# Kernel optimization log

Hardware: AMD Instinct MI355X
Metric: run time of the kernel (lower is better)

## Reference

```python
import jax, jax.numpy as jnp
import numpy as np

GELU = lambda v: jax.nn.gelu(v, approximate=False)  # torch nn.GELU default (exact erf)


def _gconv(x, w):
    # grouped conv1d, valid padding; w: (C,1,K), groups=C. lax conv = cross-correlation, same as torch.
    return jax.lax.conv_general_dilated(x, w, (1,), [(0, 0)],
                                        dimension_numbers=('NCH', 'OIH', 'NCH'),
                                        feature_group_count=x.shape[1])


def _conv(x, w, b):
    # dense conv1d, kernel 3, padding=1
    y = jax.lax.conv_general_dilated(x, w, (1,), [(1, 1)],
                                     dimension_numbers=('NCH', 'OIH', 'NCH'))
    return y + b[None, :, None]


def setup_inputs() -> dict:
    key = jax.random.key(0)
    ks = jax.random.split(key, 12)
    B, C, L = 8, 64, 2048
    H, FL, HD, TD, level = 32, 8, 64, 16, 3
    Cs = (1 + level) * C  # 256 channels into the ODE
    n = lambda k, s: (jax.random.normal(k, s) * 0.05).astype(jnp.float32)
    z = lambda s: jnp.zeros(s, jnp.float32)
    return dict(
        x=jax.random.normal(ks[0], (B, C, L), jnp.float32),
        # DyWAN_QR params
        sw1=n(ks[1], (H, C)), sb1=z((H,)),
        sw2=n(ks[2], (H, H)), sb2=z((H,)),
        sw3=n(ks[3], (2 * FL, H)), sb3=z((2 * FL,)),
        # ODE time embed / FiLM params
        tw1=n(ks[4], (TD, 1)), tb1=z((TD,)),
        tw2=n(ks[5], (TD, TD)), tb2=z((TD,)),
        cw=n(ks[6], (2 * HD, TD)), cb=z((2 * HD,)),
        # ODE conv stack params
        k1=n(ks[7], (HD, Cs, 3)), kb1=z((HD,)),
        k2=n(ks[8], (HD, HD, 3)), kb2=z((HD,)),
        k3=n(ks[9], (Cs, HD, 3)), kb3=z((Cs,)),
    )


def reference(x, sw1, sb1, sw2, sb2, sw3, sb3, tw1, tb1, tw2, tb2, cw, cb,
              k1, kb1, k2, kb2, k3, kb3):
    B, C, L = x.shape
    level, FL, T = 3, 8, 5

    def dywan(a):
        # stat_net: adaptive max pool over L -> (B,C) -> Linear -> GELU
        feat = GELU(jnp.max(a, axis=-1) @ sw1.T + sb1)
        raw = GELU(feat @ sw2.T + sb2) @ sw3.T + sb3  # (B, 2*FL)
        lo_raw, hi_raw = raw[:, :FL], raw[:, FL:]
        # QR of an (FL,1) column vector == L2 normalization (up to LAPACK sign)
        lo = lo_raw / jnp.linalg.norm(lo_raw, axis=1, keepdims=True)
        hi = hi_raw / jnp.linalg.norm(hi_raw, axis=1, keepdims=True)
        return lo, hi

    pad = FL - 1
    coeffs = [x]
    approx = x
    for _ in range(level):
        lo, hi = dywan(approx)
        lo_f = jnp.broadcast_to(lo.mean(0)[None, None, :], (C, 1, FL))
        hi_f = jnp.broadcast_to(hi.mean(0)[None, None, :], (C, 1, FL))
        ap = jnp.pad(approx, ((0, 0), (0, 0), (pad // 2, pad - pad // 2)), mode='reflect')
        new_approx = _gconv(ap, lo_f)[..., :L]
        coeffs.append(_gconv(ap, hi_f)[..., :L])
        approx = new_approx
    stacked = jnp.concatenate(coeffs, axis=1)  # (B, (1+level)*C, L)

    def ode_f(t, y):
        te = jnp.reshape(t, (1, 1)).astype(y.dtype)
        te = GELU(te @ tw1.T + tb1) @ tw2.T + tb2          # (1, TD)
        cond = te @ cw.T + cb                               # (1, 2*HD)
        hd = cond.shape[1] // 2
        gamma, beta = cond[:, :hd], cond[:, hd:]
        h = _conv(y, k1, kb1)
        h = (1.0 + gamma[:, :, None]) * h + beta[:, :, None]  # FiLM
        h = GELU(h)
        h = GELU(_conv(h, k2, kb2))
        return _conv(h, k3, kb3)

    # dopri5 tableau, fixed grid over linspace(0, 1, T) (b7 = 0, so 6 stages)
    hs = 1.0 / (T - 1)
    y = stacked
    for i in range(T - 1):
        t0 = i * hs
        s1 = ode_f(t0, y)
        s2 = ode_f(t0 + hs / 5, y + hs * (1 / 5) * s1)
        s3 = ode_f(t0 + 3 * hs / 10, y + hs * (3 / 40 * s1 + 9 / 40 * s2))
        s4 = ode_f(t0 + 4 * hs / 5, y + hs * (44 / 45 * s1 - 56 / 15 * s2 + 32 / 9 * s3))
        s5 = ode_f(t0 + 8 * hs / 9, y + hs * (19372 / 6561 * s1 - 25360 / 2187 * s2
                                              + 64448 / 6561 * s3 - 212 / 729 * s4))
        s6 = ode_f(t0 + hs, y + hs * (9017 / 3168 * s1 - 355 / 33 * s2 + 46732 / 5247 * s3
                                      + 49 / 176 * s4 - 5103 / 18656 * s5))
        y = y + hs * (35 / 384 * s1 + 500 / 1113 * s3 + 125 / 192 * s4
                      - 2187 / 6784 * s5 + 11 / 84 * s6)
    ode_out = y

    yl = ode_out[:, :C, :]
    yh0 = ode_out[:, C:2 * C, :]
    yh1 = ode_out[:, 2 * C:3 * C, :]
    yh2 = ode_out[:, 3 * C:4 * C, :]

    dx = ode_f(jnp.float32(1.0), ode_out)
    inner = jnp.sum(stacked * dx, axis=(1, 2))  # (B,)
    ecloss = jnp.mean(inner ** 2)
    return (yl, yh0, yh1, yh2, ecloss)
```

## Files before the change

### kernel.cpp

```cpp
#include <hip/hip_runtime.h>
#include <math.h>

#define B 8
#define C 64
#define L 2048
#define CS 256
#define BCL  (B*C*L)
#define BCSL (B*CS*L)
#define HS 0.25f

typedef unsigned short u16;
typedef unsigned int   u32;
typedef __attribute__((ext_vector_type(8))) short sh8;
typedef __attribute__((ext_vector_type(4))) float f4;
typedef __attribute__((ext_vector_type(8))) unsigned short us8;
typedef __attribute__((ext_vector_type(4))) unsigned short us4;

__device__ __forceinline__ float gelu(float x) {
    return 0.5f * x * (1.0f + erff(x * 0.70710678118654752440f));
}
__device__ __forceinline__ u16 f2b(float f) {
    u32 u = __float_as_uint(f);
    u32 r = u + 0x7FFFu + ((u >> 16) & 1u);
    return (u16)(r >> 16);
}
__device__ __forceinline__ float b2f(u16 h) {
    return __uint_as_float(((u32)h) << 16);
}
__device__ __forceinline__ u32 encmax(float f) {
    u32 b = __float_as_uint(f);
    return (b & 0x80000000u) ? ~b : (b | 0x80000000u);
}
__device__ __forceinline__ float decmax(u32 u) {
    return __uint_as_float((u & 0x80000000u) ? (u ^ 0x80000000u) : ~u);
}

struct ComboB { const u16* p[6]; float c[6]; };

__global__ __launch_bounds__(256) void prep_k(const float* __restrict__ w,
        u16* __restrict__ dst, int IC, int OC) {
    int idx = blockIdx.x * 256 + threadIdx.x;
    int OCG = OC >> 4;
    int j = idx & 7, lane = (idx >> 3) & 63, t = idx >> 9;
    int ocg = t % OCG, c = t / OCG;
    int oc = ocg * 16 + (lane & 15);
    int K = c * 32 + ((lane >> 4) & 3) * 8 + j;
    int kk = K / IC, ic = K % IC;
    dst[idx] = f2b(w[((size_t)oc * IC + ic) * 3 + kk]);
}

__global__ void cond25_k(const float* __restrict__ tw1, const float* __restrict__ tb1,
                         const float* __restrict__ tw2, const float* __restrict__ tb2,
                         const float* __restrict__ cw, const float* __restrict__ cb,
                         float* __restrict__ condall) {
    __shared__ float te1[16], te2[16];
    int tix = blockIdx.x;
    int tid = threadIdx.x;
    double add[6] = {0.0, 0.25/5.0, 3.0*0.25/10.0, 4.0*0.25/5.0, 8.0*0.25/9.0, 0.25};
    float t = (tix == 24) ? 1.0f : (float)((double)(tix / 6) * 0.25 + add[tix % 6]);
    if (tid < 16) te1[tid] = gelu(t * tw1[tid] + tb1[tid]);
    __syncthreads();
    if (tid < 16) {
        float s = tb2[tid];
        for (int k = 0; k < 16; ++k) s += te1[k] * tw2[tid*16+k];
        te2[tid] = s;
    }
    __syncthreads();
    float s = cb[tid];
    for (int j = 0; j < 16; ++j) s += te2[j] * cw[tid*16+j];
    condall[tix*128 + tid] = s;
}

template<int NC, int EPI>
__global__ __launch_bounds__(512) void fused_k(ComboB in,
        const u16* __restrict__ wp1, const float* __restrict__ kb1,
        const u16* __restrict__ wp2, const float* __restrict__ kb2,
        const u16* __restrict__ wp3, const float* __restrict__ kb3,
        const float* __restrict__ condall, int tix,
        u16* __restrict__ outSb,
        float* __restrict__ y, u16* __restrict__ yb,
        float* __restrict__ outp, const float* __restrict__ stacked,
        double* __restrict__ inner)
{
    __shared__ u16 xs1[50][264];
    __shared__ u16 h1t[50][72];
    __shared__ u16 h2t[34][72];
    __shared__ u16 ypart[32][264];
    __shared__ double sred[8];
    const int tid = threadIdx.x;
    const int l0  = blockIdx.x * 32;
    const int b   = blockIdx.y;
    const int g0  = l0 - 3;

    const float cy1 = HS*(35.f/384.f), cy3 = HS*(500.f/1113.f),
                cy4 = HS*(125.f/192.f), cy5 = -HS*(2187.f/6784.f),
                cy6 = HS*(11.f/84.f);

    for (int i = tid; i < 12*264; i += 512) xs1[38 + i/264][i%264] = 0;
    if (tid < 144) h1t[48 + tid/72][tid%72] = 0;

    for (int idx = tid; idx < 38*32; idx += 512) {
        int r = idx >> 5, c8 = idx & 31;
        int gl = g0 + r;
        us8 val;
        if (gl >= 0 && gl < L) {
            size_t a = ((size_t)b * L + gl) * 256 + c8 * 8;
            us8 v0 = *(const us8*)(in.p[0] + a);
            if (NC == 1) {
                val = v0;
            } else {
                float f[8];
                float yp[8];
                #pragma unroll
                for (int j = 0; j < 8; ++j) { f[j] = b2f(v0[j]); yp[j] = 0.f; }
                #pragma unroll
                for (int t = 1; t < NC; ++t) {
                    us8 vt = *(const us8*)(in.p[t] + a);
                    #pragma unroll
                    for (int j = 0; j < 8; ++j) {
                        float bv = b2f(vt[j]);
                        f[j] += in.c[t] * bv;
                        if ((EPI == 1 || EPI == 2) && (t == 1 || t == 3 || t == 4 || t == 5)) {
                            float cy = (t == 1) ? cy1 : (t == 3) ? cy3 : (t == 4) ? cy4 : cy5;
                            yp[j] += cy * bv;
                        }
                    }
                }
                #pragma unroll
                for (int j = 0; j < 8; ++j) val[j] = f2b(f[j]);
                if ((EPI == 1 || EPI == 2) && r >= 3 && r < 35) {
                    us8 ypk;
                    #pragma unroll
                    for (int j = 0; j < 8; ++j) ypk[j] = f2b(yp[j]);
                    *(us8*)&ypart[r - 3][c8 * 8] = ypk;
                }
            }
        } else {
            #pragma unroll
            for (int j = 0; j < 8; ++j) val[j] = 0;
        }
        *(us8*)&xs1[r][c8 * 8] = val;
    }
    __syncthreads();

    const int wave = tid >> 6, lane = tid & 63;
    const int nlo = lane & 15, quad = lane >> 4;

    const int ocg12  = wave & 3;
    const int nfbase = (wave < 4) ? 0 : 2;
    const int nfcnt  = (wave < 4) ? 2 : 1;

    f4 a1[2];
    a1[0] = f4{0.f,0.f,0.f,0.f}; a1[1] = a1[0];
    {
        const sh8* w1 = (const sh8*)wp1;
        for (int c = 0; c < 24; ++c) {
            int kk = c >> 3, ic0 = (c & 7) << 5;
            sh8 A = w1[(c*4 + ocg12)*64 + lane];
            #pragma unroll
            for (int k = 0; k < 2; ++k) {
                if (k < nfcnt) {
                    int nf = nfbase + k;
                    sh8 Bv = *(const sh8*)&xs1[nf*16 + nlo + kk][ic0 + quad*8];
                    a1[k] = __builtin_amdgcn_mfma_f32_16x16x32_bf16(A, Bv, a1[k], 0, 0, 0);
                }
            }
        }
    }
    {
        const float* cd = condall + tix*128;
        const int oc0 = ocg12*16 + quad*4;
        #pragma unroll
        for (int k = 0; k < 2; ++k) {
            if (k < nfcnt) {
                int nf = nfbase + k;
                int p = nf*16 + nlo;
                int gp = l0 - 2 + p;
                bool ok = (p < 36) && (gp >= 0) && (gp < L);
                us4 pk;
                #pragma unroll
                for (int reg = 0; reg < 4; ++reg) {
                    int oc = oc0 + reg;
                    float v = (1.f + cd[oc]) * (a1[k][reg] + kb1[oc]) + cd[64+oc];
                    pk[reg] = ok ? f2b(gelu(v)) : (u16)0;
                }
                *(us4*)&h1t[p][oc0] = pk;
            }
        }
    }
    __syncthreads();

    f4 a2[2];
    a2[0] = f4{0.f,0.f,0.f,0.f}; a2[1] = a2[0];
    {
        const sh8* w2 = (const sh8*)wp2;
        #pragma unroll
        for (int c = 0; c < 6; ++c) {
            int kk = c >> 1, ic0 = (c & 1) << 5;
            sh8 A = w2[(c*4 + ocg12)*64 + lane];
            #pragma unroll
            for (int k = 0; k < 2; ++k) {
                if (k < nfcnt) {
                    int nf = nfbase + k;
                    sh8 Bv = *(const sh8*)&h1t[nf*16 + nlo + kk][ic0 + quad*8];
                    a2[k] = __builtin_amdgcn_mfma_f32_16x16x32_bf16(A, Bv, a2[k], 0, 0, 0);
                }
            }
        }
    }
    {
        const int oc0 = ocg12*16 + quad*4;
        #pragma unroll
        for (int k = 0; k < 2; ++k) {
            if (k < nfcnt) {
                int nf = nfbase + k;
                int q = nf*16 + nlo;
                if (q < 34) {
                    int gq = l0 - 1 + q;
                    bool ok = (gq >= 0) && (gq < L);
                    us4 pk;
                    #pragma unroll
                    for (int reg = 0; reg < 4; ++reg)
                        pk[reg] = ok ? f2b(gelu(a2[k][reg] + kb2[oc0 + reg])) : (u16)0;
                    *(us4*)&h2t[q][oc0] = pk;
                }
            }
        }
    }
    __syncthreads();

    f4 a3[2][2];
    #pragma unroll
    for (int mf = 0; mf < 2; ++mf) { a3[mf][0] = f4{0.f,0.f,0.f,0.f}; a3[mf][1] = a3[mf][0]; }
    {
        const sh8* w3 = (const sh8*)wp3;
        #pragma unroll
        for (int c = 0; c < 6; ++c) {
            int kk = c >> 1, ic0 = (c & 1) << 5;
            sh8 B0 = *(const sh8*)&h2t[nlo + kk][ic0 + quad*8];
            sh8 B1 = *(const sh8*)&h2t[16 + nlo + kk][ic0 + quad*8];
            #pragma unroll
            for (int mf = 0; mf < 2; ++mf) {
                sh8 A = w3[(c*16 + wave*2 + mf)*64 + lane];
                a3[mf][0] = __builtin_amdgcn_mfma_f32_16x16x32_bf16(A, B0, a3[mf][0], 0, 0, 0);
                a3[mf][1] = __builtin_amdgcn_mfma_f32_16x16x32_bf16(A, B1, a3[mf][1], 0, 0, 0);
            }
        }
    }

    if (EPI == 3) {
        double acc = 0.0;
        #pragma unroll
        for (int mf = 0; mf < 2; ++mf)
            #pragma unroll
            for (int nf = 0; nf < 2; ++nf) {
                int pos = l0 + nf*16 + nlo;
                #pragma unroll
                for (int reg = 0; reg < 4; ++reg) {
                    int oc = (wave*2 + mf)*16 + quad*4 + reg;
                    size_t idx = ((size_t)b*CS + oc)*L + pos;
                    float dx = a3[mf][nf][reg] + kb3[oc];
                    acc += (double)stacked[idx] * (double)dx;
                }
            }
        #pragma unroll
        for (int off = 32; off > 0; off >>= 1) acc += __shfl_down(acc, off, 64);
        if (lane == 0) sred[wave] = acc;
        __syncthreads();
        if (tid == 0) {
            double s = 0.0;
            #pragma unroll
            for (int w = 0; w < 8; ++w) s += sred[w];
            atomicAdd(&inner[b], s);
        }
    } else if (EPI == 0) {
        #pragma unroll
        for (int mf = 0; mf < 2; ++mf) {
            int baseoc = (wave*2 + mf)*16 + quad*4;
            #pragma unroll
            for (int nf = 0; nf < 2; ++nf) {
                int pos = l0 + nf*16 + nlo;
                us4 pk;
                #pragma unroll
                for (int reg = 0; reg < 4; ++reg)
                    pk[reg] = f2b(a3[mf][nf][reg] + kb3[baseoc + reg]);
                *(us4*)(outSb + ((size_t)b*L + pos)*256 + baseoc) = pk;
            }
        }
    } else {
        #pragma unroll
        for (int mf = 0; mf < 2; ++mf) {
            int baseoc = (wave*2 + mf)*16 + quad*4;
            #pragma unroll
            for (int nf = 0; nf < 2; ++nf) {
                int pl = nf*16 + nlo;
                int pos = l0 + pl;
                us4 yp4 = *(const us4*)&ypart[pl][baseoc];
                us4 pk;
                #pragma unroll
                for (int reg = 0; reg < 4; ++reg) {
                    int oc = baseoc + reg;
                    size_t idx = ((size_t)b*CS + oc)*L + pos;
                    float s6 = a3[mf][nf][reg] + kb3[oc];
                    float yv = y[idx] + b2f(yp4[reg]) + cy6 * s6;
                    pk[reg] = f2b(yv);
                    if (EPI == 1) y[idx] = yv;
                    if (EPI == 2) {
                        size_t oidx = (((size_t)(oc >> 6)*B + b)*64 + (oc & 63))*L + pos;
                        outp[oidx] = yv;
                    }
                }
                *(us4*)(yb + ((size_t)b*L + pos)*256 + baseoc) = pk;
            }
        }
    }
}

__global__ __launch_bounds__(256) void mlp_k(const u32* __restrict__ bm,
    const float* __restrict__ sw1, const float* __restrict__ sb1,
    const float* __restrict__ sw2, const float* __restrict__ sb2,
    const float* __restrict__ sw3, const float* __restrict__ sb3,
    float* __restrict__ filt) {
    __shared__ float m[8][64], f1[8][32], f2[8][32], raw[8][16], nrm[8][2];
    int tid = threadIdx.x;
    for (int i = tid; i < 512; i += 256) m[i >> 6][i & 63] = decmax(bm[i]);
    __syncthreads();
    {
        int b = tid >> 5, h = tid & 31;
        float s = sb1[h];
        for (int c = 0; c < 64; ++c) s += m[b][c] * sw1[h*64+c];
        f1[b][h] = gelu(s);
    }
    __syncthreads();
    {
        int b = tid >> 5, h = tid & 31;
        float s = sb2[h];
        for (int k = 0; k < 32; ++k) s += f1[b][k] * sw2[h*32+k];
        f2[b][h] = gelu(s);
    }
    __syncthreads();
    if (tid < 128) {
        int b = tid >> 4, j = tid & 15;
        float s = sb3[j];
        for (int k = 0; k < 32; ++k) s += f2[b][k] * sw3[j*32+k];
        raw[b][j] = s;
    }
    __syncthreads();
    if (tid < 16) {
        int b = tid >> 1, half = tid & 1;
        float s = 0.f;
        for (int j = 0; j < 8; ++j) { float v = raw[b][half*8+j]; s += v*v; }
        nrm[b][half] = sqrtf(s);
    }
    __syncthreads();
    if (tid < 16) {
        int half = tid >> 3;
        float s = 0.f;
        for (int b = 0; b < 8; ++b) s += raw[b][tid] / nrm[b][half];
        filt[tid] = s * 0.125f;
    }
}

__global__ __launch_bounds__(256) void wconv_k(const float* __restrict__ ap,
    const float* __restrict__ filt, float* __restrict__ apOut,
    float* __restrict__ stacked, int lev, u32* __restrict__ bmaxn) {
    __shared__ float f[16];
    __shared__ float red[256];
    if (threadIdx.x < 16) f[threadIdx.x] = filt[threadIdx.x];
    __syncthreads();
    size_t idx = (size_t)blockIdx.x * 256 + threadIdx.x;
    int l = (int)(idx & 2047);
    size_t bc = idx >> 11;
    int c = (int)(bc & 63), b = (int)(bc >> 6);
    const float* row = ap + (bc << 11);
    float lo = 0.f, hi = 0.f;
    #pragma unroll
    for (int k = 0; k < 8; ++k) {
        int mI = l + k - 3;
        mI = mI < 0 ? -mI : (mI >= L ? 2*L - 2 - mI : mI);
        float v = row[mI];
        lo += v * f[k];
        hi += v * f[8+k];
    }
    stacked[((size_t)b * CS + (size_t)(lev+1) * 64 + c) * L + l] = hi;
    if (bmaxn) {
        apOut[idx] = lo;
        red[threadIdx.x] = lo;
        __syncthreads();
        for (int s = 128; s > 0; s >>= 1) {
            if (threadIdx.x < s) red[threadIdx.x] = fmaxf(red[threadIdx.x], red[threadIdx.x + s]);
            __syncthreads();
        }
        if (threadIdx.x == 0) atomicMax(&bmaxn[blockIdx.x >> 3], encmax(red[0]));
    }
}

__global__ __launch_bounds__(256) void copyx_k(const float* __restrict__ x,
        float* __restrict__ st, u32* __restrict__ bmax0) {
    __shared__ float red[256];
    size_t i = (size_t)blockIdx.x * 256 + threadIdx.x;
    size_t b = i >> 17, rem = i & 131071;
    float v = x[i];
    st[b * ((size_t)CS*L) + rem] = v;
    red[threadIdx.x] = v;
    __syncthreads();
    for (int s = 128; s > 0; s >>= 1) {
        if (threadIdx.x < s) red[threadIdx.x] = fmaxf(red[threadIdx.x], red[threadIdx.x + s]);
        __syncthreads();
    }
    if (threadIdx.x == 0) atomicMax(&bmax0[blockIdx.x >> 3], encmax(red[0]));
}

__global__ __launch_bounds__(256) void tinit_k(const float* __restrict__ st,
        float* __restrict__ y, u16* __restrict__ yb) {
    __shared__ float t[64][65];
    const int tid = threadIdx.x;
    const int l0 = blockIdx.x * 64, c0 = blockIdx.y * 64, b = blockIdx.z;
    #pragma unroll
    for (int k = 0; k < 16; ++k) {
        int c = k * 4 + (tid >> 6), l = tid & 63;
        size_t idx = ((size_t)b*CS + c0 + c) * L + l0 + l;
        float v = st[idx];
        y[idx] = v;
        t[c][l] = v;
    }
    __syncthreads();
    #pragma unroll
    for (int k = 0; k < 16; ++k) {
        int p = k * 4 + (tid >> 6), ch = tid & 63;
        yb[((size_t)b * L + l0 + p) * 256 + c0 + ch] = f2b(t[ch][p]);
    }
}

__global__ void ecfin_k(const double* __restrict__ inner, float* __restrict__ out) {
    double s = 0.0;
    for (int b = 0; b < 8; ++b) s += inner[b] * inner[b];
    out[BCSL] = (float)(s / 8.0);
}

extern "C" void kernel_launch(void* const* d_in, const int* in_sizes, int n_in,
                              void* d_out, int out_size, void* d_ws, size_t ws_size,
                              hipStream_t stream) {
    const float* x   = (const float*)d_in[0];
    const float* sw1 = (const float*)d_in[1];
    const float* sb1 = (const float*)d_in[2];
    const float* sw2 = (const float*)d_in[3];
    const float* sb2 = (const float*)d_in[4];
    const float* sw3 = (const float*)d_in[5];
    const float* sb3 = (const float*)d_in[6];
    const float* tw1 = (const float*)d_in[7];
    const float* tb1 = (const float*)d_in[8];
    const float* tw2 = (const float*)d_in[9];
    const float* tb2 = (const float*)d_in[10];
    const float* cw  = (const float*)d_in[11];
    const float* cb  = (const float*)d_in[12];
    const float* k1  = (const float*)d_in[13];
    const float* kb1 = (const float*)d_in[14];
    const float* k2  = (const float*)d_in[15];
    const float* kb2 = (const float*)d_in[16];
    const float* k3  = (const float*)d_in[17];
    const float* kb3 = (const float*)d_in[18];
    float* out = (float*)d_out;

    char* cur = (char*)d_ws;
    auto alloc = [&](size_t bytes) { void* p = cur; cur += (bytes + 255) & ~(size_t)255; return p; };
    float* stacked = (float*)alloc(BCSL * 4);
    float* y       = (float*)alloc(BCSL * 4);
    u16*   yb      = (u16*)  alloc(BCSL * 2);
    u16*   sbuf[5];
    for (int i = 0; i < 5; ++i) sbuf[i] = (u16*)alloc(BCSL * 2);
    float* cond  = (float*)alloc(3200 * 4);
    double* inner = (double*)alloc(8 * 8);
    u32* bmaxe   = (u32*)alloc(3 * 512 * 4);
    float* filt  = (float*)alloc(16 * 4);
    u16* wp1 = (u16*)alloc(49152 * 2);
    u16* wp2 = (u16*)alloc(12288 * 2);
    u16* wp3 = (u16*)alloc(49152 * 2);

    u16 *s1b = sbuf[0], *s2b = sbuf[1], *s3b = sbuf[2], *s4b = sbuf[3], *s5b = sbuf[4];

    hipMemsetAsync(inner, 0, 256 + 3 * 512 * 4, stream);

    prep_k<<<192, 256, 0, stream>>>(k1, wp1, CS, C);
    prep_k<<<48,  256, 0, stream>>>(k2, wp2, C,  C);
    prep_k<<<192, 256, 0, stream>>>(k3, wp3, C,  CS);
    cond25_k<<<25, 128, 0, stream>>>(tw1, tb1, tw2, tb2, cw, cb, cond);

    copyx_k<<<4096, 256, 0, stream>>>(x, stacked, bmaxe);
    const float* apIn = x;
    float* apBuf[2] = {(float*)s1b, (float*)s2b};
    for (int lev = 0; lev < 3; ++lev) {
        mlp_k<<<1, 256, 0, stream>>>(bmaxe + lev*512, sw1, sb1, sw2, sb2, sw3, sb3, filt);
        float* apOut = apBuf[lev & 1];
        wconv_k<<<4096, 256, 0, stream>>>(apIn, filt, apOut, stacked, lev,
                                          (lev < 2) ? (bmaxe + (lev+1)*512) : nullptr);
        apIn = apOut;
    }
    tinit_k<<<dim3(32, 4, 8), 256, 0, stream>>>(stacked, y, yb);

    const float hs = HS;
    dim3 cg(64, 8);
    #define LAUNCH(NC, EPI, CIN, TIX, OUTSB, OUTP, STK) \
        fused_k<NC, EPI><<<cg, 512, 0, stream>>>(CIN, wp1, kb1, wp2, kb2, wp3, kb3, \
            cond, TIX, OUTSB, y, yb, OUTP, STK, inner)

    for (int i = 0; i < 4; ++i) {
        ComboB cA{}; cA.p[0] = yb;
        LAUNCH(1, 0, cA, i*6+0, s1b, nullptr, nullptr);

        ComboB cB{}; cB.p[0] = yb; cB.p[1] = s1b; cB.c[1] = hs*(1.f/5.f);
        LAUNCH(2, 0, cB, i*6+1, s2b, nullptr, nullptr);

        ComboB cC{}; cC.p[0] = yb;
        cC.p[1] = s1b; cC.c[1] = hs*(3.f/40.f);
        cC.p[2] = s2b; cC.c[2] = hs*(9.f/40.f);
        LAUNCH(3, 0, cC, i*6+2, s3b, nullptr, nullptr);

        ComboB cD{}; cD.p[0] = yb;
        cD.p[1] = s1b; cD.c[1] = hs*(44.f/45.f);
        cD.p[2] = s2b; cD.c[2] = -hs*(56.f/15.f);
        cD.p[3] = s3b; cD.c[3] = hs*(32.f/9.f);
        LAUNCH(4, 0, cD, i*6+3, s4b, nullptr, nullptr);

        ComboB cE{}; cE.p[0] = yb;
        cE.p[1] = s1b; cE.c[1] = hs*(19372.f/6561.f);
        cE.p[2] = s2b; cE.c[2] = -hs*(25360.f/2187.f);
        cE.p[3] = s3b; cE.c[3] = hs*(64448.f/6561.f);
        cE.p[4] = s4b; cE.c[4] = -hs*(212.f/729.f);
        LAUNCH(5, 0, cE, i*6+4, s5b, nullptr, nullptr);

        ComboB cF{}; cF.p[0] = yb;
        cF.p[1] = s1b; cF.c[1] = hs*(9017.f/3168.f);
        cF.p[2] = s2b; cF.c[2] = -hs*(355.f/33.f);
        cF.p[3] = s3b; cF.c[3] = hs*(46732.f/5247.f);
        cF.p[4] = s4b; cF.c[4] = hs*(49.f/176.f);
        cF.p[5] = s5b; cF.c[5] = -hs*(5103.f/18656.f);
        if (i < 3) {
            LAUNCH(6, 1, cF, i*6+5, nullptr, nullptr, nullptr);
        } else {
            LAUNCH(6, 2, cF, i*6+5, nullptr, out, nullptr);
        }
    }

    ComboB cZ{}; cZ.p[0] = yb;
    LAUNCH(1, 3, cZ, 24, nullptr, nullptr, stacked);
    ecfin_k<<<1, 1, 0, stream>>>(inner, out);
    #undef LAUNCH
}
```

Baseline: 696.0 us.

## Fuse RK stages into two kernels per step using halo recomputation

After: 859.3 us. 23.5% more time.

```diff
diff --git a/kernel.cpp b/kernel.cpp
--- a/kernel.cpp
+++ b/kernel.cpp
@@ -34,8 +34,6 @@
 __device__ __forceinline__ float decmax(u32 u) {
     return __uint_as_float((u & 0x80000000u) ? (u ^ 0x80000000u) : ~u);
 }
-
-struct ComboB { const u16* p[6]; float c[6]; };
 
 __global__ __launch_bounds__(256) void prep_k(const float* __restrict__ w,
         u16* __restrict__ dst, int IC, int OC) {
@@ -71,248 +69,491 @@
     condall[tix*128 + tid] = s;
 }
 
-template<int NC, int EPI>
-__global__ __launch_bounds__(512) void fused_k(ComboB in,
+
+template<int NF>
+__device__ __forceinline__ void do_conv1(const u16* __restrict__ wp1,
+        const float* __restrict__ kb1, const float* __restrict__ cd,
+        const u16 (*__restrict__ IN)[264], u16 (*__restrict__ H1)[72],
+        int n_valid, int gp0, int wave, int lane)
+{
+    const int nlo = lane & 15, quad = lane >> 4;
+    const int ocg = wave & 3;
+    const int nf0 = (NF == 3) ? ((wave < 4) ? 0 : 2) : (wave >> 2);
+    const int nfc = (NF == 3) ? ((wave < 4) ? 2 : 1) : 1;
+    f4 acc[2];
+    acc[0] = f4{0.f,0.f,0.f,0.f}; acc[1] = acc[0];
+    const sh8* w1 = (const sh8*)wp1;
+    for (int c = 0; c < 24; ++c) {
+        int kk = c >> 3, ic0 = (c & 7) << 5;
+        sh8 A = w1[(c*4 + ocg)*64 + lane];
+        #pragma unroll
+        for (int k = 0; k < 2; ++k) {
+            if (k < nfc) {
+                int nf = nf0 + k;
+                sh8 Bv = *(const sh8*)&IN[nf*16 + nlo + kk][ic0 + quad*8];
+                acc[k] = __builtin_amdgcn_mfma_f32_16x16x32_bf16(A, Bv, acc[k], 0, 0, 0);
+            }
+        }
+    }
+    const int oc0 = ocg*16 + quad*4;
+    #pragma unroll
+    for (int k = 0; k < 2; ++k) {
+        if (k < nfc) {
+            int nf = nf0 + k;
+            int p = nf*16 + nlo;
+            int gp = gp0 + p;
+            bool ok = (p < n_valid) && (gp >= 0) && (gp < L);
+            us4 pk;
+            #pragma unroll
+            for (int reg = 0; reg < 4; ++reg) {
+                int oc = oc0 + reg;
+                float v = (1.f + cd[oc]) * (acc[k][reg] + kb1[oc]) + cd[64+oc];
+                pk[reg] = ok ? f2b(gelu(v)) : (u16)0;
+            }
+            *(us4*)&H1[p][oc0] = pk;
+        }
+    }
+}
+
+template<int NF>
+__device__ __forceinline__ void do_conv2(const u16* __restrict__ wp2,
+        const float* __restrict__ kb2,
+        const u16 (*__restrict__ H1)[72], u16 (*__restrict__ H2)[72],
+        int n_valid, int gq0, int wave, int lane)
+{
+    const int nlo = lane & 15, quad = lane >> 4;
+    const int ocg = wave & 3;
+    const int nf0 = (NF == 3) ? ((wave < 4) ? 0 : 2) : (wave >> 2);
+    const int nfc = (NF == 3) ? ((wave < 4) ? 2 : 1) : 1;
+    f4 acc[2];
+    acc[0] = f4{0.f,0.f,0.f,0.f}; acc[1] = acc[0];
+    const sh8* w2 = (const sh8*)wp2;
+    #pragma unroll
+    for (int c = 0; c < 6; ++c) {
+        int kk = c >> 1, ic0 = (c & 1) << 5;
+        sh8 A = w2[(c*4 + ocg)*64 + lane];
+        #pragma unroll
+        for (int k = 0; k < 2; ++k) {
+            if (k < nfc) {
+                int nf = nf0 + k;
+                sh8 Bv = *(const sh8*)&H1[nf*16 + nlo + kk][ic0 + quad*8];
+                acc[k] = __builtin_amdgcn_mfma_f32_16x16x32_bf16(A, Bv, acc[k], 0, 0, 0);
+            }
+        }
+    }
+    const int oc0 = ocg*16 + quad*4;
+    #pragma unroll
+    for (int k = 0; k < 2; ++k) {
+        if (k < nfc) {
+            int nf = nf0 + k;
+            int q = nf*16 + nlo;
+            int gq = gq0 + q;
+            bool ok = (q < n_valid) && (gq >= 0) && (gq < L);
+            us4 pk;
+            #pragma unroll
+            for (int reg = 0; reg < 4; ++reg)
+                pk[reg] = ok ? f2b(gelu(acc[k][reg] + kb2[oc0 + reg])) : (u16)0;
+            *(us4*)&H2[q][oc0] = pk;
+        }
+    }
+}
+
+template<int NFO>
+__device__ __forceinline__ void do_conv3(const u16* __restrict__ wp3,
+        const u16 (*__restrict__ H2)[72], f4 (&acc)[2][3], int wave, int lane)
+{
+    const int nlo = lane & 15, quad = lane >> 4;
+    #pragma unroll
+    for (int mf = 0; mf < 2; ++mf)
+        #pragma unroll
+        for (int nf = 0; nf < NFO; ++nf) acc[mf][nf] = f4{0.f,0.f,0.f,0.f};
+    const sh8* w3 = (const sh8*)wp3;
+    #pragma unroll
+    for (int c = 0; c < 6; ++c) {
+        int kk = c >> 1, ic0 = (c & 1) << 5;
+        sh8 Bf[3];
+        #pragma unroll
+        for (int nf = 0; nf < NFO; ++nf)
+            Bf[nf] = *(const sh8*)&H2[nf*16 + nlo + kk][ic0 + quad*8];
+        #pragma unroll
+        for (int mf = 0; mf < 2; ++mf) {
+            sh8 A = w3[(c*16 + wave*2 + mf)*64 + lane];
+            #pragma unroll
+            for (int nf = 0; nf < NFO; ++nf)
+                acc[mf][nf] = __builtin_amdgcn_mfma_f32_16x16x32_bf16(A, Bf[nf], acc[mf][nf], 0, 0, 0);
+        }
+    }
+}
+
+template<int NFO>
+__device__ __forceinline__ void store_S(const f4 (&a)[2][3], u16 (*__restrict__ S)[264],
+        int nrow, int gm0, u16* __restrict__ gout, int b, int gw0, int gw1,
+        const float* __restrict__ kb3, int wave, int lane)
+{
+    const int nlo = lane & 15, quad = lane >> 4;
+    #pragma unroll
+    for (int mf = 0; mf < 2; ++mf) {
+        const int oc0 = (wave*2 + mf)*16 + quad*4;
+        #pragma unroll
+        for (int nf = 0; nf < NFO; ++nf) {
+            const int m = nf*16 + nlo;
+            const int gm = gm0 + m;
+            const bool ok = (gm >= 0) && (gm < L);
+            us4 pk;
+            #pragma unroll
+            for (int reg = 0; reg < 4; ++reg)
+                pk[reg] = ok ? f2b(a[mf][nf][reg] + kb3[oc0 + reg]) : (u16)0;
+            if (S != nullptr && m < nrow) *(us4*)&S[m][oc0] = pk;
+            if (gout != nullptr && m >= gw0 && m < gw1)
+                *(us4*)(gout + ((size_t)b*L + gm)*256 + oc0) = pk;
+        }
+    }
+}
+
+__global__ __launch_bounds__(512) void kA_k(const u16* __restrict__ ybin,
         const u16* __restrict__ wp1, const float* __restrict__ kb1,
         const u16* __restrict__ wp2, const float* __restrict__ kb2,
         const u16* __restrict__ wp3, const float* __restrict__ kb3,
-        const float* __restrict__ condall, int tix,
-        u16* __restrict__ outSb,
-        float* __restrict__ y, u16* __restrict__ yb,
-        float* __restrict__ outp, const float* __restrict__ stacked,
-        double* __restrict__ inner)
+        const float* __restrict__ condall, int tix0,
+        u16* __restrict__ s1g, u16* __restrict__ s2g, u16* __restrict__ s3g)
 {
-    __shared__ u16 xs1[50][264];
-    __shared__ u16 h1t[50][72];
-    __shared__ u16 h2t[34][72];
-    __shared__ u16 ypart[32][264];
-    __shared__ double sred[8];
-    const int tid = threadIdx.x;
-    const int l0  = blockIdx.x * 32;
-    const int b   = blockIdx.y;
-    const int g0  = l0 - 3;
-
+    __shared__ u16 Y[50][264];
+    __shared__ u16 S1[44][264];
+    __shared__ u16 S2[38][264];
+    __shared__ u16 CB[50][264];
+    __shared__ u16 H1[50][72];
+    __shared__ u16 H2[50][72];
+    const int tid = threadIdx.x, wave = tid >> 6, lane = tid & 63;
+    const int l0 = blockIdx.x * 32, b = blockIdx.y;
+    const int g0 = l0 - 9;
+
+    if (tid < 144) H1[48 + tid/72][tid%72] = 0;
+    else if (tid < 288) { int t = tid - 144; H2[48 + t/72][t%72] = 0; }
+
+    for (int idx = tid; idx < 50*32; idx += 512) {
+        int r = idx >> 5, o = (idx & 31) * 8;
+        int gl = g0 + r;
+        us8 v;
+        if (gl >= 0 && gl < L) {
+            v = *(const us8*)(ybin + ((size_t)b*L + gl)*256 + o);
+        } else {
+            #pragma unroll
+            for (int j = 0; j < 8; ++j) v[j] = 0;
+        }
+        *(us8*)&Y[r][o] = v;
+    }
+    __syncthreads();
+
+    do_conv1<3>(wp1, kb1, condall + (tix0+0)*128, Y, H1, 48, l0-8, wave, lane);
+    __syncthreads();
+    do_conv2<3>(wp2, kb2, H1, H2, 46, l0-7, wave, lane);
+    __syncthreads();
+    {
+        f4 a[2][3];
+        do_conv3<3>(wp3, H2, a, wave, lane);
+        store_S<3>(a, S1, 44, l0-6, s1g, b, 6, 38, kb3, wave, lane);
+    }
+    __syncthreads();
+
+    {
+        const float cB1 = HS*(1.f/5.f);
+        for (int idx = tid; idx < 44*32; idx += 512) {
+            int r = idx >> 5, o = (idx & 31) * 8;
+            us8 vy = *(const us8*)&Y[r+3][o];
+            us8 v1 = *(const us8*)&S1[r][o];
+            us8 ov;
+            #pragma unroll
+            for (int j = 0; j < 8; ++j) {
+                float f = b2f(vy[j]);
+                f += cB1 * b2f(v1[j]);
+                ov[j] = f2b(f);
+            }
+            *(us8*)&CB[r][o] = ov;
+        }
+    }
+    __syncthreads();
+
+    do_conv1<3>(wp1, kb1, condall + (tix0+1)*128, CB, H1, 42, l0-5, wave, lane);
+    __syncthreads();
+    do_conv2<3>(wp2, kb2, H1, H2, 40, l0-4, wave, lane);
+    __syncthreads();
+    {
+        f4 a[2][3];
+        do_conv3<3>(wp3, H2, a, wave, lane);
+        store_S<3>(a, S2, 38, l0-3, s2g, b, 3, 35, kb3, wave, lane);
+    }
+    __syncthreads();
+
+    {
+        const float cC1 = HS*(3.f/40.f), cC2 = HS*(9.f/40.f);
+        for (int idx = tid; idx < 38*32; idx += 512) {
+            int r = idx >> 5, o = (idx & 31) * 8;
+            us8 vy = *(const us8*)&Y[r+6][o];
+            us8 v1 = *(const us8*)&S1[r+3][o];
+            us8 v2 = *(const us8*)&S2[r][o];
+            us8 ov;
+            #pragma unroll
+            for (int j = 0; j < 8; ++j) {
+                float f = b2f(vy[j]);
+                f += cC1 * b2f(v1[j]);
+                f += cC2 * b2f(v2[j]);
+                ov[j] = f2b(f);
+            }
+            *(us8*)&CB[r][o] = ov;
+        }
+    }
+    __syncthreads();
+
+    do_conv1<3>(wp1, kb1, condall + (tix0+2)*128, CB, H1, 36, l0-2, wave, lane);
+    __syncthreads();
+    do_conv2<3>(wp2, kb2, H1, H2, 34, l0-1, wave, lane);
+    __syncthreads();
+    {
+        f4 a[2][3];
+        do_conv3<2>(wp3, H2, a, wave, lane);
+        store_S<2>(a, (u16(*)[264])nullptr, 0, l0, s3g, b, 0, 32, kb3, wave, lane);
+    }
+}
+
+template<int EPI>
+__global__ __launch_bounds__(512) void kB_k(const u16* __restrict__ ybin,
+        const u16* __restrict__ s1g, const u16* __restrict__ s2g, const u16* __restrict__ s3g,
+        const u16* __restrict__ wp1, const float* __restrict__ kb1,
+        const u16* __restrict__ wp2, const float* __restrict__ kb2,
+        const u16* __restrict__ wp3, const float* __restrict__ kb3,
+        const float* __restrict__ condall, int tix0,
+        float* __restrict__ y, u16* __restrict__ ybout, float* __restrict__ outp)
+{
+    __shared__ u16 Y[34][264], S1[34][264], S2[34][264], S3[34][264];
+    __shared__ u16 CB[34][264], S4[28][264], S5[24][264];
+    __shared__ u16 H1[34][72], H2[34][72];
+    const int tid = threadIdx.x, wave = tid >> 6, lane = tid & 63;
+    const int l0 = blockIdx.x * 16, b = blockIdx.y;
+    const int g0 = l0 - 9;
     const float cy1 = HS*(35.f/384.f), cy3 = HS*(500.f/1113.f),
                 cy4 = HS*(125.f/192.f), cy5 = -HS*(2187.f/6784.f),
                 cy6 = HS*(11.f/84.f);
 
-    for (int i = tid; i < 12*264; i += 512) xs1[38 + i/264][i%264] = 0;
-    if (tid < 144) h1t[48 + tid/72][tid%72] = 0;
+    if (tid < 144) H1[32 + tid/72][tid%72] = 0;
+    else if (tid < 288) { int t = tid - 144; H2[32 + t/72][t%72] = 0; }
+
+    for (int idx = tid; idx < 34*32; idx += 512) {
+        int r = idx >> 5, o = (idx & 31) * 8;
+        int gl = g0 + r;
+        us8 vy, v1, v2, v3;
+        if (gl >= 0 && gl < L) {
+            size_t adr = ((size_t)b*L + gl)*256 + o;
+            vy = *(const us8*)(ybin + adr);
+            v1 = *(const us8*)(s1g + adr);
+            v2 = *(const us8*)(s2g + adr);
+            v3 = *(const us8*)(s3g + adr);
+        } else {
+            #pragma unroll
+            for (int j = 0; j < 8; ++j) { vy[j] = 0; v1[j] = 0; v2[j] = 0; v3[j] = 0; }
+        }
+        *(us8*)&Y[r][o] = vy;
+        *(us8*)&S1[r][o] = v1;
+        *(us8*)&S2[r][o] = v2;
+        *(us8*)&S3[r][o] = v3;
+    }
+    __syncthreads();
+
+    {
+        const float cD1 = HS*(44.f/45.f), cD2 = -HS*(56.f/15.f), cD3 = HS*(32.f/9.f);
+        for (int idx = tid; idx < 34*32; idx += 512) {
+            int r = idx >> 5, o = (idx & 31) * 8;
+            us8 vy = *(const us8*)&Y[r][o];
+            us8 v1 = *(const us8*)&S1[r][o];
+            us8 v2 = *(const us8*)&S2[r][o];
+            us8 v3 = *(const us8*)&S3[r][o];
+            us8 ov;
+            #pragma unroll
+            for (int j = 0; j < 8; ++j) {
+                float f = b2f(vy[j]);
+                f += cD1 * b2f(v1[j]);
+                f += cD2 * b2f(v2[j]);
+                f += cD3 * b2f(v3[j]);
+                ov[j] = f2b(f);
+            }
+            *(us8*)&CB[r][o] = ov;
+        }
+    }
+    __syncthreads();
+    do_conv1<2>(wp1, kb1, condall + (tix0+0)*128, CB, H1, 32, l0-8, wave, lane);
+    __syncthreads();
+    do_conv2<2>(wp2, kb2, H1, H2, 30, l0-7, wave, lane);
+    __syncthreads();
+    {
+        f4 a[2][3];
+        do_conv3<2>(wp3, H2, a, wave, lane);
+        store_S<2>(a, S4, 28, l0-6, (u16*)nullptr, b, 0, 0, kb3, wave, lane);
+    }
+    __syncthreads();
+
+    {
+        const float cE1 = HS*(19372.f/6561.f), cE2 = -HS*(25360.f/2187.f),
+                    cE3 = HS*(64448.f/6561.f), cE4 = -HS*(212.f/729.f);
+        for (int idx = tid; idx < 28*32; idx += 512) {
+            int r = idx >> 5, o = (idx & 31) * 8;
+            us8 vy = *(const us8*)&Y[r+3][o];
+            us8 v1 = *(const us8*)&S1[r+3][o];
+            us8 v2 = *(const us8*)&S2[r+3][o];
+            us8 v3 = *(const us8*)&S3[r+3][o];
+            us8 v4 = *(const us8*)&S4[r][o];
+            us8 ov;
+            #pragma unroll
+            for (int j = 0; j < 8; ++j) {
+                float f = b2f(vy[j]);
+                f += cE1 * b2f(v1[j]);
+                f += cE2 * b2f(v2[j]);
+                f += cE3 * b2f(v3[j]);
+                f += cE4 * b2f(v4[j]);
+                ov[j] = f2b(f);
+            }
+            *(us8*)&CB[r][o] = ov;
+        }
+    }
+    __syncthreads();
+    do_conv1<2>(wp1, kb1, condall + (tix0+1)*128, CB, H1, 26, l0-5, wave, lane);
+    __syncthreads();
+    do_conv2<2>(wp2, kb2, H1, H2, 24, l0-4, wave, lane);
+    __syncthreads();
+    {
+        f4 a[2][3];
+        do_conv3<2>(wp3, H2, a, wave, lane);
+        store_S<2>(a, S5, 22, l0-3, (u16*)nullptr, b, 0, 0, kb3, wave, lane);
+    }
+    __syncthreads();
+
+    {
+        const float cF1 = HS*(9017.f/3168.f), cF2 = -HS*(355.f/33.f),
+                    cF3 = HS*(46732.f/5247.f), cF4 = HS*(49.f/176.f),
+                    cF5 = -HS*(5103.f/18656.f);
+        for (int idx = tid; idx < 22*32; idx += 512) {
+            int r = idx >> 5, o = (idx & 31) * 8;
+            us8 vy = *(const us8*)&Y[r+6][o];
+            us8 v1 = *(const us8*)&S1[r+6][o];
+            us8 v2 = *(const us8*)&S2[r+6][o];
+            us8 v3 = *(const us8*)&S3[r+6][o];
+            us8 v4 = *(const us8*)&S4[r+3][o];
+            us8 v5 = *(const us8*)&S5[r][o];
+            us8 ov;
+            #pragma unroll
+            for (int j = 0; j < 8; ++j) {
+                float f = b2f(vy[j]);
+                f += cF1 * b2f(v1[j]);
+                f += cF2 * b2f(v2[j]);
+                f += cF3 * b2f(v3[j]);
+                f += cF4 * b2f(v4[j]);
+                f += cF5 * b2f(v5[j]);
+                ov[j] = f2b(f);
+            }
+            *(us8*)&CB[r][o] = ov;
+        }
+    }
+    __syncthreads();
+    do_conv1<2>(wp1, kb1, condall + (tix0+2)*128, CB, H1, 20, l0-2, wave, lane);
+    __syncthreads();
+    do_conv2<2>(wp2, kb2, H1, H2, 18, l0-1, wave, lane);
+    __syncthreads();
+    f4 a[2][3];
+    do_conv3<1>(wp3, H2, a, wave, lane);
+
+    const int nlo = lane & 15, quad = lane >> 4;
+    const int pos = l0 + nlo;
+    #pragma unroll
+    for (int mf = 0; mf < 2; ++mf) {
+        const int oc0 = (wave*2 + mf)*16 + quad*4;
+        us4 v1 = *(const us4*)&S1[nlo + 9][oc0];
+        us4 v3 = *(const us4*)&S3[nlo + 9][oc0];
+        us4 v4 = *(const us4*)&S4[nlo + 6][oc0];
+        us4 v5 = *(const us4*)&S5[nlo + 3][oc0];
+        us4 pk;
+        #pragma unroll
+        for (int reg = 0; reg < 4; ++reg) {
+            int oc = oc0 + reg;
+            float yp = cy1 * b2f(v1[reg]);
+            yp += cy3 * b2f(v3[reg]);
+            yp += cy4 * b2f(v4[reg]);
+            yp += cy5 * b2f(v5[reg]);
+            u16 ypb = f2b(yp);
+            float s6 = a[mf][0][reg] + kb3[oc];
+            size_t idx = ((size_t)b*CS + oc)*L + pos;
+            float yv = y[idx] + b2f(ypb) + cy6 * s6;
+            pk[reg] = f2b(yv);
+            if (EPI == 1) y[idx] = yv;
+            else {
+                size_t oidx = (((size_t)(oc >> 6)*B + b)*64 + (oc & 63))*L + pos;
+                outp[oidx] = yv;
+            }
+        }
+        *(us4*)(ybout + ((size_t)b*L + pos)*256 + oc0) = pk;
+    }
+}
+
+__global__ __launch_bounds__(512) void ec_k(const u16* __restrict__ ybin,
+        const u16* __restrict__ wp1, const float* __restrict__ kb1,
+        const u16* __restrict__ wp2, const float* __restrict__ kb2,
+        const u16* __restrict__ wp3, const float* __restrict__ kb3,
+        const float* __restrict__ condall,
+        const float* __restrict__ stacked, double* __restrict__ inner)
+{
+    __shared__ u16 XS[50][264];
+    __shared__ u16 H1[50][72];
+    __shared__ u16 H2[50][72];
+    __shared__ double sred[8];
+    const int tid = threadIdx.x, wave = tid >> 6, lane = tid & 63;
+    const int l0 = blockIdx.x * 32, b = blockIdx.y;
+    const int g0 = l0 - 3;
+
+    for (int i = tid; i < 12*264; i += 512) XS[38 + i/264][i%264] = 0;
+    if (tid < 144) H1[48 + tid/72][tid%72] = 0;
+    else if (tid < 288) { int t = tid - 144; H2[48 + t/72][t%72] = 0; }
 
     for (int idx = tid; idx < 38*32; idx += 512) {
-        int r = idx >> 5, c8 = idx & 31;
+        int r = idx >> 5, o = (idx & 31) * 8;
         int gl = g0 + r;
-        us8 val;
+        us8 v;
         if (gl >= 0 && gl < L) {
-            size_t a = ((size_t)b * L + gl) * 256 + c8 * 8;
-            us8 v0 = *(const us8*)(in.p[0] + a);
-            if (NC == 1) {
-                val = v0;
-            } else {
-                float f[8];
-                float yp[8];
-                #pragma unroll
-                for (int j = 0; j < 8; ++j) { f[j] = b2f(v0[j]); yp[j] = 0.f; }
-                #pragma unroll
-                for (int t = 1; t < NC; ++t) {
-                    us8 vt = *(const us8*)(in.p[t] + a);
-                    #pragma unroll
-                    for (int j = 0; j < 8; ++j) {
-                        float bv = b2f(vt[j]);
-                        f[j] += in.c[t] * bv;
-                        if ((EPI == 1 || EPI == 2) && (t == 1 || t == 3 || t == 4 || t == 5)) {
-                            float cy = (t == 1) ? cy1 : (t == 3) ? cy3 : (t == 4) ? cy4 : cy5;
-                            yp[j] += cy * bv;
-                        }
-                    }
-                }
-                #pragma unroll
-                for (int j = 0; j < 8; ++j) val[j] = f2b(f[j]);
-                if ((EPI == 1 || EPI == 2) && r >= 3 && r < 35) {
-                    us8 ypk;
-                    #pragma unroll
-                    for (int j = 0; j < 8; ++j) ypk[j] = f2b(yp[j]);
-                    *(us8*)&ypart[r - 3][c8 * 8] = ypk;
-                }
-            }
+            v = *(const us8*)(ybin + ((size_t)b*L + gl)*256 + o);
         } else {
             #pragma unroll
-            for (int j = 0; j < 8; ++j) val[j] = 0;
-        }
-        *(us8*)&xs1[r][c8 * 8] = val;
-    }
-    __syncthreads();
-
-    const int wave = tid >> 6, lane = tid & 63;
+            for (int j = 0; j < 8; ++j) v[j] = 0;
+        }
+        *(us8*)&XS[r][o] = v;
+    }
+    __syncthreads();
+    do_conv1<3>(wp1, kb1, condall + 24*128, XS, H1, 36, l0-2, wave, lane);
+    __syncthreads();
+    do_conv2<3>(wp2, kb2, H1, H2, 34, l0-1, wave, lane);
+    __syncthreads();
+    f4 a[2][3];
+    do_conv3<2>(wp3, H2, a, wave, lane);
+
     const int nlo = lane & 15, quad = lane >> 4;
-
-    const int ocg12  = wave & 3;
-    const int nfbase = (wave < 4) ? 0 : 2;
-    const int nfcnt  = (wave < 4) ? 2 : 1;
-
-    f4 a1[2];
-    a1[0] = f4{0.f,0.f,0.f,0.f}; a1[1] = a1[0];
-    {
-        const sh8* w1 = (const sh8*)wp1;
-        for (int c = 0; c < 24; ++c) {
-            int kk = c >> 3, ic0 = (c & 7) << 5;
-            sh8 A = w1[(c*4 + ocg12)*64 + lane];
-            #pragma unroll
-            for (int k = 0; k < 2; ++k) {
-                if (k < nfcnt) {
-                    int nf = nfbase + k;
-                    sh8 Bv = *(const sh8*)&xs1[nf*16 + nlo + kk][ic0 + quad*8];
-                    a1[k] = __builtin_amdgcn_mfma_f32_16x16x32_bf16(A, Bv, a1[k], 0, 0, 0);
-                }
-            }
-        }
-    }
-    {
-        const float* cd = condall + tix*128;
-        const int oc0 = ocg12*16 + quad*4;
-        #pragma unroll
-        for (int k = 0; k < 2; ++k) {
-            if (k < nfcnt) {
-                int nf = nfbase + k;
-                int p = nf*16 + nlo;
-                int gp = l0 - 2 + p;
-                bool ok = (p < 36) && (gp >= 0) && (gp < L);
-                us4 pk;
-                #pragma unroll
-                for (int reg = 0; reg < 4; ++reg) {
-                    int oc = oc0 + reg;
-                    float v = (1.f + cd[oc]) * (a1[k][reg] + kb1[oc]) + cd[64+oc];
-                    pk[reg] = ok ? f2b(gelu(v)) : (u16)0;
-                }
-                *(us4*)&h1t[p][oc0] = pk;
-            }
-        }
-    }
-    __syncthreads();
-
-    f4 a2[2];
-    a2[0] = f4{0.f,0.f,0.f,0.f}; a2[1] = a2[0];
-    {
-        const sh8* w2 = (const sh8*)wp2;
-        #pragma unroll
-        for (int c = 0; c < 6; ++c) {
-            int kk = c >> 1, ic0 = (c & 1) << 5;
-            sh8 A = w2[(c*4 + ocg12)*64 + lane];
-            #pragma unroll
-            for (int k = 0; k < 2; ++k) {
-                if (k < nfcnt) {
-                    int nf = nfbase + k;
-                    sh8 Bv = *(const sh8*)&h1t[nf*16 + nlo + kk][ic0 + quad*8];
-                    a2[k] = __builtin_amdgcn_mfma_f32_16x16x32_bf16(A, Bv, a2[k], 0, 0, 0);
-                }
-            }
-        }
-    }
-    {
-        const int oc0 = ocg12*16 + quad*4;
-        #pragma unroll
-        for (int k = 0; k < 2; ++k) {
-            if (k < nfcnt) {
-                int nf = nfbase + k;
-                int q = nf*16 + nlo;
-                if (q < 34) {
-                    int gq = l0 - 1 + q;
-                    bool ok = (gq >= 0) && (gq < L);
-                    us4 pk;
-                    #pragma unroll
-                    for (int reg = 0; reg < 4; ++reg)
-                        pk[reg] = ok ? f2b(gelu(a2[k][reg] + kb2[oc0 + reg])) : (u16)0;
-                    *(us4*)&h2t[q][oc0] = pk;
-                }
-            }
-        }
-    }
-    __syncthreads();
-
-    f4 a3[2][2];
-    #pragma unroll
-    for (int mf = 0; mf < 2; ++mf) { a3[mf][0] = f4{0.f,0.f,0.f,0.f}; a3[mf][1] = a3[mf][0]; }
-    {
-        const sh8* w3 = (const sh8*)wp3;
-        #pragma unroll
-        for (int c = 0; c < 6; ++c) {
-            int kk = c >> 1, ic0 = (c & 1) << 5;
-            sh8 B0 = *(const sh8*)&h2t[nlo + kk][ic0 + quad*8];
-            sh8 B1 = *(const sh8*)&h2t[16 + nlo + kk][ic0 + quad*8];
-            #pragma unroll
-            for (int mf = 0; mf < 2; ++mf) {
-                sh8 A = w3[(c*16 + wave*2 + mf)*64 + lane];
-                a3[mf][0] = __builtin_amdgcn_mfma_f32_16x16x32_bf16(A, B0, a3[mf][0], 0, 0, 0);
-                a3[mf][1] = __builtin_amdgcn_mfma_f32_16x16x32_bf16(A, B1, a3[mf][1], 0, 0, 0);
-            }
-        }
-    }
-
-    if (EPI == 3) {
-        double acc = 0.0;
-        #pragma unroll
-        for (int mf = 0; mf < 2; ++mf)
-            #pragma unroll
-            for (int nf = 0; nf < 2; ++nf) {
-                int pos = l0 + nf*16 + nlo;
-                #pragma unroll
-                for (int reg = 0; reg < 4; ++reg) {
-                    int oc = (wave*2 + mf)*16 + quad*4 + reg;
-                    size_t idx = ((size_t)b*CS + oc)*L + pos;
-                    float dx = a3[mf][nf][reg] + kb3[oc];
-                    acc += (double)stacked[idx] * (double)dx;
-                }
-            }
-        #pragma unroll
-        for (int off = 32; off > 0; off >>= 1) acc += __shfl_down(acc, off, 64);
-        if (lane == 0) sred[wave] = acc;
-        __syncthreads();
-        if (tid == 0) {
-            double s = 0.0;
-            #pragma unroll
-            for (int w = 0; w < 8; ++w) s += sred[w];
-            atomicAdd(&inner[b], s);
-        }
-    } else if (EPI == 0) {
-        #pragma unroll
-        for (int mf = 0; mf < 2; ++mf) {
-            int baseoc = (wave*2 + mf)*16 + quad*4;
-            #pragma unroll
-            for (int nf = 0; nf < 2; ++nf) {
-                int pos = l0 + nf*16 + nlo;
-                us4 pk;
-                #pragma unroll
-                for (int reg = 0; reg < 4; ++reg)
-                    pk[reg] = f2b(a3[mf][nf][reg] + kb3[baseoc + reg]);
-                *(us4*)(outSb + ((size_t)b*L + pos)*256 + baseoc) = pk;
-            }
-        }
-    } else {
-        #pragma unroll
-        for (int mf = 0; mf < 2; ++mf) {
-            int baseoc = (wave*2 + mf)*16 + quad*4;
-            #pragma unroll
-            for (int nf = 0; nf < 2; ++nf) {
-                int pl = nf*16 + nlo;
-                int pos = l0 + pl;
-                us4 yp4 = *(const us4*)&ypart[pl][baseoc];
-                us4 pk;
-                #pragma unroll
-                for (int reg = 0; reg < 4; ++reg) {
-                    int oc = baseoc + reg;
-                    size_t idx = ((size_t)b*CS + oc)*L + pos;
-                    float s6 = a3[mf][nf][reg] + kb3[oc];
-                    float yv = y[idx] + b2f(yp4[reg]) + cy6 * s6;
-                    pk[reg] = f2b(yv);
-                    if (EPI == 1) y[idx] = yv;
-                    if (EPI == 2) {
-                        size_t oidx = (((size_t)(oc >> 6)*B + b)*64 + (oc & 63))*L + pos;
-                        outp[oidx] = yv;
-                    }
-                }
-                *(us4*)(yb + ((size_t)b*L + pos)*256 + baseoc) = pk;
-            }
-        }
+    double acc = 0.0;
+    #pragma unroll
+    for (int mf = 0; mf < 2; ++mf)
+        #pragma unroll
+        for (int nf = 0; nf < 2; ++nf) {
+            int pos = l0 + nf*16 + nlo;
+            #pragma unroll
+            for (int reg = 0; reg < 4; ++reg) {
+                int oc = (wave*2 + mf)*16 + quad*4 + reg;
+                size_t idx = ((size_t)b*CS + oc)*L + pos;
+                float dx = a[mf][nf][reg] + kb3[oc];
+                acc += (double)stacked[idx] * (double)dx;
+            }
+        }
+    #pragma unroll
+    for (int off = 32; off > 0; off >>= 1) acc += __shfl_down(acc, off, 64);
+    if (lane == 0) sred[wave] = acc;
+    __syncthreads();
+    if (tid == 0) {
+        double s = 0.0;
+        #pragma unroll
+        for (int w = 0; w < 8; ++w) s += sred[w];
+        atomicAdd(&inner[b], s);
     }
 }
 
@@ -466,9 +707,11 @@
     auto alloc = [&](size_t bytes) { void* p = cur; cur += (bytes + 255) & ~(size_t)255; return p; };
     float* stacked = (float*)alloc(BCSL * 4);
     float* y       = (float*)alloc(BCSL * 4);
-    u16*   yb      = (u16*)  alloc(BCSL * 2);
-    u16*   sbuf[5];
-    for (int i = 0; i < 5; ++i) sbuf[i] = (u16*)alloc(BCSL * 2);
+    u16*   yba     = (u16*)  alloc(BCSL * 2);
+    u16*   ybb     = (u16*)  alloc(BCSL * 2);
+    u16*   s1b     = (u16*)  alloc(BCSL * 2);
+    u16*   s2b     = (u16*)  alloc(BCSL * 2);
+    u16*   s3b     = (u16*)  alloc(BCSL * 2);
     float* cond  = (float*)alloc(3200 * 4);
     double* inner = (double*)alloc(8 * 8);
     u32* bmaxe   = (u32*)alloc(3 * 512 * 4);
@@ -476,8 +719,6 @@
     u16* wp1 = (u16*)alloc(49152 * 2);
     u16* wp2 = (u16*)alloc(12288 * 2);
     u16* wp3 = (u16*)alloc(49152 * 2);
-
-    u16 *s1b = sbuf[0], *s2b = sbuf[1], *s3b = sbuf[2], *s4b = sbuf[3], *s5b = sbuf[4];
 
     hipMemsetAsync(inner, 0, 256 + 3 * 512 * 4, stream);
 
@@ -496,54 +737,23 @@
                                           (lev < 2) ? (bmaxe + (lev+1)*512) : nullptr);
         apIn = apOut;
     }
-    tinit_k<<<dim3(32, 4, 8), 256, 0, stream>>>(stacked, y, yb);
-
-    const float hs = HS;
-    dim3 cg(64, 8);
-    #define LAUNCH(NC, EPI, CIN, TIX, OUTSB, OUTP, STK) \
-        fused_k<NC, EPI><<<cg, 512, 0, stream>>>(CIN, wp1, kb1, wp2, kb2, wp3, kb3, \
-            cond, TIX, OUTSB, y, yb, OUTP, STK, inner)
-
+    tinit_k<<<dim3(32, 4, 8), 256, 0, stream>>>(stacked, y, yba);
+
+    u16* ybs[2] = {yba, ybb};
     for (int i = 0; i < 4; ++i) {
-        ComboB cA{}; cA.p[0] = yb;
-        LAUNCH(1, 0, cA, i*6+0, s1b, nullptr, nullptr);
-
-        ComboB cB{}; cB.p[0] = yb; cB.p[1] = s1b; cB.c[1] = hs*(1.f/5.f);
-        LAUNCH(2, 0, cB, i*6+1, s2b, nullptr, nullptr);
-
-        ComboB cC{}; cC.p[0] = yb;
-        cC.p[1] = s1b; cC.c[1] = hs*(3.f/40.f);
-        cC.p[2] = s2b; cC.c[2] = hs*(9.f/40.f);
-        LAUNCH(3, 0, cC, i*6+2, s3b, nullptr, nullptr);
-
-        ComboB cD{}; cD.p[0] = yb;
-        cD.p[1] = s1b; cD.c[1] = hs*(44.f/45.f);
-        cD.p[2] = s2b; cD.c[2] = -hs*(56.f/15.f);
-        cD.p[3] = s3b; cD.c[3] = hs*(32.f/9.f);
-        LAUNCH(4, 0, cD, i*6+3, s4b, nullptr, nullptr);
-
-        ComboB cE{}; cE.p[0] = yb;
-        cE.p[1] = s1b; cE.c[1] = hs*(19372.f/6561.f);
-        cE.p[2] = s2b; cE.c[2] = -hs*(25360.f/2187.f);
-        cE.p[3] = s3b; cE.c[3] = hs*(64448.f/6561.f);
-        cE.p[4] = s4b; cE.c[4] = -hs*(212.f/729.f);
-        LAUNCH(5, 0, cE, i*6+4, s5b, nullptr, nullptr);
-
-        ComboB cF{}; cF.p[0] = yb;
-        cF.p[1] = s1b; cF.c[1] = hs*(9017.f/3168.f);
-        cF.p[2] = s2b; cF.c[2] = -hs*(355.f/33.f);
-        cF.p[3] = s3b; cF.c[3] = hs*(46732.f/5247.f);
-        cF.p[4] = s4b; cF.c[4] = hs*(49.f/176.f);
-        cF.p[5] = s5b; cF.c[5] = -hs*(5103.f/18656.f);
-        if (i < 3) {
-            LAUNCH(6, 1, cF, i*6+5, nullptr, nullptr, nullptr);
-        } else {
-            LAUNCH(6, 2, cF, i*6+5, nullptr, out, nullptr);
-        }
-    }
-
-    ComboB cZ{}; cZ.p[0] = yb;
-    LAUNCH(1, 3, cZ, 24, nullptr, nullptr, stacked);
+        const u16* ybr = ybs[i & 1];
+        u16* ybw = ybs[(i & 1) ^ 1];
+        kA_k<<<dim3(64, 8), 512, 0, stream>>>(ybr, wp1, kb1, wp2, kb2, wp3, kb3,
+                                              cond, i*6, s1b, s2b, s3b);
+        if (i < 3)
+            kB_k<1><<<dim3(128, 8), 512, 0, stream>>>(ybr, s1b, s2b, s3b,
+                    wp1, kb1, wp2, kb2, wp3, kb3, cond, i*6+3, y, ybw, nullptr);
+        else
+            kB_k<2><<<dim3(128, 8), 512, 0, stream>>>(ybr, s1b, s2b, s3b,
+                    wp1, kb1, wp2, kb2, wp3, kb3, cond, i*6+3, y, ybw, out);
+    }
+
+    ec_k<<<dim3(64, 8), 512, 0, stream>>>(ybs[0], wp1, kb1, wp2, kb2, wp3, kb3,
+                                          cond, stacked, inner);
     ecfin_k<<<1, 1, 0, stream>>>(inner, out);
-    #undef LAUNCH
-}
+}
```
